# Kernel optimization log

Hardware: AMD Instinct MI355X
Metric: run time of the kernel (lower is better)

The kernel has to match this reference:

```python
import jax, jax.numpy as jnp
import numpy as np
from jax import lax

H_SIZE = 2048; ATT = 512; HEAD = 64
H = H_SIZE // HEAD; HK = ATT // HEAD; G = H // HK
D_DECAY = 96; D_AAA = 96; D_MV = 64; D_GATE = 256
B, T = 1, 2048
EPS = 1e-5 * HEAD  # ln_x eps = 1e-5 * head_size


def setup_inputs() -> dict:
    ks = jax.random.split(jax.random.key(0), 32)
    f = jnp.float32
    rn = lambda k, sh, s: jax.random.normal(k, sh, dtype=f) * s
    return {
        "x": rn(ks[0], (B, T, H_SIZE), 1.0),
        "wkv_state_in": jnp.zeros((B, H, HEAD, HEAD), f),
        "v_first_val": rn(ks[1], (B, T, H_SIZE), 1.0),
        "cos": jax.random.uniform(ks[2], (T, HEAD), dtype=f),
        "sin": jax.random.uniform(ks[3], (T, HEAD), dtype=f),
        "w0": rn(ks[4], (1, 1, H_SIZE), 0.3) - 2.0,
        "w1": rn(ks[5], (H_SIZE, D_DECAY), 0.02),
        "w2": rn(ks[6], (D_DECAY, H_SIZE), 0.05),
        "a0": rn(ks[7], (1, 1, H_SIZE), 0.1),
        "a1": rn(ks[8], (H_SIZE, D_AAA), 0.02),
        "a2": rn(ks[9], (D_AAA, H_SIZE), 0.05),
        "v0": jnp.ones((1, 1, H_SIZE), f),
        "v1": rn(ks[10], (H_SIZE, D_MV), 0.02),
        "v2": rn(ks[11], (D_MV, H_SIZE), 0.05),
        "g1": rn(ks[12], (H_SIZE, D_GATE), 0.02),
        "g2": rn(ks[13], (D_GATE, H_SIZE), 0.05),
        "k_k": jnp.full((1, 1, H_SIZE), 0.85, f),
        "k_a": jnp.ones((1, 1, H_SIZE), f),
        "r_k": rn(ks[14], (H, HEAD), 0.2),
        "q_w": rn(ks[15], (H_SIZE, H_SIZE), 0.02), "q_b": rn(ks[16], (H_SIZE,), 0.02),
        "k_w": rn(ks[17], (ATT, H_SIZE), 0.02), "k_b": rn(ks[18], (ATT,), 0.02),
        "v_w": rn(ks[19], (ATT, H_SIZE), 0.02), "v_b": rn(ks[20], (ATT,), 0.02),
        "o_w": rn(ks[21], (H_SIZE, H_SIZE), 0.02),
        "ln_w": jnp.ones((H_SIZE,), f), "ln_b": jnp.zeros((H_SIZE,), f),
    }


def _rope(x4, cos, sin):
    # x4: [B,T,h,N], cos/sin: [T,N]; HF rotate_half convention
    c = cos[None, :, None, :]; s = sin[None, :, None, :]
    x1, x2 = jnp.split(x4, 2, axis=-1)
    return x4 * c + jnp.concatenate([-x2, x1], axis=-1) * s


def _forward(x, wkv_state_in, v_first_val, cos, sin, w0, w1, w2, a0, a1, a2,
             v0, v1, v2, g1, g2, k_k, k_a, r_k, q_w, q_b, k_w, k_b, v_w, v_b,
             o_w, ln_w, ln_b):
    Bx, Tx, C = x.shape
    r = x @ q_w.T + q_b                                   # [B,T,C]
    w_lora = w0 + jnp.tanh(x @ w1) @ w2                   # [B,T,C]
    k = x @ k_w.T + k_b                                   # [B,T,ATT]
    v = x @ v_w.T + v_b                                   # [B,T,ATT]
    g = jax.nn.sigmoid(x @ g1) @ g2                       # [B,T,C]
    iclr = jax.nn.sigmoid(a0 + (x @ a1) @ a2)             # in-context learning rate

    r4 = _rope(r.reshape(Bx, Tx, H, HEAD), cos, sin)
    k4 = _rope(k.reshape(Bx, Tx, HK, HEAD), cos, sin)
    # GQA expand kv heads to all query heads
    k4 = jnp.repeat(k4, G, axis=2)                        # [B,T,H,N]
    v4 = jnp.repeat(v.reshape(Bx, Tx, HK, HEAD), G, axis=2)
    v = v4.reshape(Bx, Tx, C)
    # v_first residual mix (layer_id > 0)
    v = v + (v_first_val - v) * jax.nn.sigmoid(v0 + (x @ v1) @ v2)
    k = k4.reshape(Bx, Tx, C)
    kk = (k * k_k).reshape(Bx, Tx, H, HEAD)
    kk = kk / jnp.maximum(jnp.linalg.norm(kk, axis=-1, keepdims=True), 1e-12)
    k = k * (1.0 + (iclr - 1.0) * k_a)
    # decay: soft-clamped log-decay then double-exp -> (0,1)
    w = jnp.exp(-jnp.exp(-jax.nn.softplus(-w_lora) - 0.5))

    tm = lambda a: jnp.moveaxis(a.reshape(Bx, Tx, H, HEAD), 1, 0)  # time-major [T,B,H,N]
    seq = (tm(r4.reshape(Bx, Tx, C)), tm(w), tm(k), tm(v),
           jnp.moveaxis(kk, 1, 0), tm(iclr))

    def step(S, inp):
        r_t, w_t, k_t, v_t, kk_t, a_t = inp
        ab = kk_t * a_t
        S = (S * w_t[:, :, None, :]
             + jnp.einsum('bhij,bhj,bhk->bhik', S, -kk_t, ab)
             + v_t[..., None] * k_t[:, :, None, :])
        y = jnp.einsum('bhij,bhj->bhi', S, r_t)
        return S, y

    S_out, ys = lax.scan(step, wkv_state_in.astype(jnp.float32), seq)
    y = jnp.moveaxis(ys, 0, 1)                            # [B,T,H,N]
    # GroupNorm(n_head) per token
    mu = y.mean(-1, keepdims=True)
    var = y.var(-1)[..., None]
    y = (y - mu) / jnp.sqrt(var + EPS)
    y = y.reshape(Bx, Tx, C) * ln_w + ln_b
    # per-head bonus term
    bonus = (r4 * k.reshape(Bx, Tx, H, HEAD) * r_k).sum(-1, keepdims=True) \
            * v.reshape(Bx, Tx, H, HEAD)
    y = y + bonus.reshape(Bx, Tx, C)
    out = (y * g) @ o_w.T
    return out, S_out, v_first_val


def reference(x, wkv_state_in, v_first_val, cos, sin, w0, w1, w2, a0, a1, a2,
              v0, v1, v2, g1, g2, k_k, k_a, r_k, q_w, q_b, k_w, k_b, v_w, v_b,
              o_w, ln_w, ln_b):
    return _forward(x, wkv_state_in, v_first_val, cos, sin, w0, w1, w2, a0, a1,
                    a2, v0, v1, v2, g1, g2, k_k, k_a, r_k, q_w, q_b, k_w, k_b,
                    v_w, v_b, o_w, ln_w, ln_b)
```

## Files before the change

kernel.cpp:

```cpp
#include <hip/hip_runtime.h>
#include <hip/hip_bf16.h>

typedef __hip_bfloat16 bf16;
typedef unsigned int u32;
typedef __attribute__((ext_vector_type(8))) __bf16 bf16x8;
typedef __attribute__((ext_vector_type(4))) float f32x4;
typedef __attribute__((ext_vector_type(8))) short short8;

static constexpr int kT   = 2048;
static constexpr int kC   = 2048;
static constexpr int kAtt = 512;

__device__ __forceinline__ float us2f(unsigned short u) {
    union { float f; unsigned int i; } c; c.i = ((unsigned int)u) << 16; return c.f;
}
__device__ __forceinline__ float toF(float v) { return v; }
__device__ __forceinline__ float toF(bf16 v) { return __bfloat162float(v); }
__device__ __forceinline__ void stO(float* p, float v) { *p = v; }
__device__ __forceinline__ void stO(bf16* p, float v) { *p = __float2bfloat16(v); }
__device__ __forceinline__ unsigned short f2us(float x) {
    return __builtin_bit_cast(unsigned short, __float2bfloat16(x));
}
__device__ __forceinline__ u32 packbf(float lo, float hi) {
    return (u32)f2us(lo) | ((u32)f2us(hi) << 16);
}

__device__ __forceinline__ void ld4(const bf16* p, float r[4]) {
    ushort4 u = *reinterpret_cast<const ushort4*>(p);
    r[0] = us2f(u.x); r[1] = us2f(u.y); r[2] = us2f(u.z); r[3] = us2f(u.w);
}
__device__ __forceinline__ void ld4(const float* p, float r[4]) {
    float4 u = *reinterpret_cast<const float4*>(p);
    r[0] = u.x; r[1] = u.y; r[2] = u.z; r[3] = u.w;
}

__device__ __forceinline__ float wred64(float v) {
    #pragma unroll
    for (int m = 32; m > 0; m >>= 1) v += __shfl_xor(v, m, 64);
    return v;
}

__device__ __forceinline__ void gload_lds16(const bf16* g, void* lds) {
    __builtin_amdgcn_global_load_lds(
        (const __attribute__((address_space(1))) void*)g,
        (__attribute__((address_space(3))) void*)lds, 16, 0, 0);
}

__global__ void detect_kernel(const unsigned short* __restrict__ v0,
                              int* __restrict__ flag) {
    if (threadIdx.x == 0) flag[0] = (v0[0] == 0x3F80) ? 0 : 1;
}

struct ConvDesc { const void* src; void* dst; int n; int b0; };
struct ConvTable { ConvDesc d[12]; };

__global__ __launch_bounds__(256) void conv_all(const int* __restrict__ flag,
                                                ConvTable tab) {
    const bool isf = flag[0] != 0;
    const int bid = blockIdx.x;
    int di = 0;
    #pragma unroll
    for (int k = 1; k < 12; k++) if (bid >= tab.d[k].b0) di = k;
    const ConvDesc d = tab.d[di];
    const int i = ((bid - d.b0) * 256 + threadIdx.x) * 4;
    if (i >= d.n) return;
    float r[4];
    if (isf) ld4((const float*)d.src + i, r);
    else     ld4((const bf16*)d.src + i, r);
    bf16* o = (bf16*)d.dst;
    ushort4 o4 = { f2us(r[0]), f2us(r[1]), f2us(r[2]), f2us(r[3]) };
    *reinterpret_cast<ushort4*>(o + i) = o4;
}

struct TransDesc { const void* src; void* dst; int R, C, b0; };
struct TransTable { TransDesc d[8]; };

__global__ __launch_bounds__(256) void trans_all(const int* __restrict__ flag,
                                                 TransTable tab) {
    const bool isf = flag[0] != 0;
    const int bid = blockIdx.x;
    int di = 0;
    #pragma unroll
    for (int k = 1; k < 8; k++) if (bid >= tab.d[k].b0) di = k;
    const TransDesc d = tab.d[di];
    const int tC = d.C >> 5;
    const int tile = bid - d.b0;
    const int by = tile / tC, bx = tile - by * tC;
    __shared__ float tilebuf[32][33];
    const int r0 = by << 5, c0 = bx << 5;
    const int x = threadIdx.x & 31, y4 = (threadIdx.x >> 5) << 2;
    if (isf) {
        const float* src = (const float*)d.src;
        #pragma unroll
        for (int k = 0; k < 4; k++)
            tilebuf[y4 + k][x] = src[(size_t)(r0 + y4 + k) * d.C + c0 + x];
    } else {
        const bf16* src = (const bf16*)d.src;
        #pragma unroll
        for (int k = 0; k < 4; k++)
            tilebuf[y4 + k][x] = toF(src[(size_t)(r0 + y4 + k) * d.C + c0 + x]);
    }
    __syncthreads();
    bf16* dst = (bf16*)d.dst;
    #pragma unroll
    for (int k = 0; k < 4; k++)
        dst[(size_t)(c0 + y4 + k) * d.R + r0 + x] = __float2bfloat16(tilebuf[x][y4 + k]);
}

template<typename OT, int BM, int BN>
__device__ __forceinline__ void gemm_body(
    bf16* As, bf16* Bs,
    const bf16* __restrict__ A, int lda, const bf16* __restrict__ B,
    const bf16* __restrict__ bias, OT* __restrict__ C,
    int N, int K, int epi)
{
    const int tid = threadIdx.x, lane = tid & 63, wave = tid >> 6;
    const int bm = blockIdx.y * BM, bn = blockIdx.x * BN;
    const int wm = (wave >> 1) * (BM / 2), wn = (wave & 1) * (BN / 2);
    constexpr int FI = BM / 32, FJ = BN / 32;
    f32x4 acc[FI][FJ];
    #pragma unroll
    for (int i = 0; i < FI; i++)
        #pragma unroll
        for (int j = 0; j < FJ; j++) acc[i][j] = (f32x4){0.f, 0.f, 0.f, 0.f};
    const int sr = tid >> 2;
    const int sc = (tid & 3) << 3;
    const int fr = lane & 15;
    const int fk = (lane >> 4) << 3;
    char* AsB = (char*)As + wave * 1024;
    char* BsB = (char*)Bs + wave * 1024;
    for (int k0 = 0; k0 < K; k0 += 32) {
        #pragma unroll
        for (int it = 0; it < BM / 64; it++)
            gload_lds16(A + (size_t)(bm + sr + it * 64) * lda + k0 + sc,
                        AsB + it * 4096);
        #pragma unroll
        for (int it = 0; it < BN / 64; it++)
            gload_lds16(B + (size_t)(bn + sr + it * 64) * K + k0 + sc,
                        BsB + it * 4096);
        __syncthreads();
        bf16x8 af[FI], bg[FJ];
        #pragma unroll
        for (int f = 0; f < FI; f++)
            af[f] = *reinterpret_cast<const bf16x8*>(&As[(wm + f * 16 + fr) * 32 + fk]);
        #pragma unroll
        for (int f = 0; f < FJ; f++)
            bg[f] = *reinterpret_cast<const bf16x8*>(&Bs[(wn + f * 16 + fr) * 32 + fk]);
        #pragma unroll
        for (int fi = 0; fi < FI; fi++)
            #pragma unroll
            for (int fj = 0; fj < FJ; fj++)
                acc[fi][fj] = __builtin_amdgcn_mfma_f32_16x16x32_bf16(
                    af[fi], bg[fj], acc[fi][fj], 0, 0, 0);
        __syncthreads();
    }
    #pragma unroll
    for (int fi = 0; fi < FI; fi++) {
        const int m = bm + wm + fi * 16 + ((lane >> 4) << 2);
        #pragma unroll
        for (int fj = 0; fj < FJ; fj++) {
            const int n = bn + wn + fj * 16 + (lane & 15);
            #pragma unroll
            for (int e = 0; e < 4; e++) {
                float v = acc[fi][fj][e];
                if (epi == 1 || epi == 2 || epi == 3) v += toF(bias[n]);
                if (epi == 2) v = 1.f / (1.f + expf(-v));
                if (epi == 3) {
                    v = 1.f / (1.f + expf(-v));
                    v = 1.f - expf(-0.6065306597126334f * v);
                }
                if (epi == 6) {
                    if (n < 96) v = tanhf(v);
                    else if (n >= 256) v = 1.f / (1.f + expf(-v));
                }
                stO(&C[(size_t)(m + e) * N + n], v);
            }
        }
    }
}

template<typename OT, int EPI, int BM, int BN>
__global__ __launch_bounds__(256) void mfma_nt(
    const bf16* __restrict__ A, int lda, const bf16* __restrict__ B,
    const bf16* __restrict__ bias, OT* __restrict__ C, int N, int K)
{
    __shared__ bf16 As[BM * 32];
    __shared__ bf16 Bs[BN * 32];
    gemm_body<OT, BM, BN>(As, Bs, A, lda, B, bias, C, N, K, EPI);
}

struct L2Desc { const bf16* A; const bf16* B; const bf16* bias; bf16* C; int K; int epi; };
struct L2Table { L2Desc d[4]; };

__global__ __launch_bounds__(256) void lora2_all(L2Table tab) {
    __shared__ bf16 As[128 * 32];
    __shared__ bf16 Bs[128 * 32];
    const L2Desc d = tab.d[blockIdx.z];
    gemm_body<bf16, 128, 128>(As, Bs, d.A, 512, d.B, d.bias, d.C, kC, d.K, d.epi);
}

__global__ __launch_bounds__(256) void out_all(
    const int* __restrict__ flag, const bf16* __restrict__ A,
    const bf16* __restrict__ B, bf16* __restrict__ Cb, float* __restrict__ Cf)
{
    __shared__ bf16 As[128 * 32];
    __shared__ bf16 Bs[128 * 32];
    if (flag[0]) gemm_body<float, 128, 128>(As, Bs, A, kC, B, nullptr, Cf, kC, kC, 0);
    else         gemm_body<bf16, 128, 128>(As, Bs, A, kC, B, nullptr, Cb, kC, kC, 0);
}

template<typename IT>
__device__ __forceinline__ void prep_body(
    const bf16* __restrict__ rkv, const bf16* __restrict__ iclr,
    const bf16* __restrict__ wdec, bf16* __restrict__ vout,
    const IT* __restrict__ vfirst, const IT* __restrict__ cosw,
    const IT* __restrict__ sinw, const IT* __restrict__ kkw,
    const IT* __restrict__ kaw, const IT* __restrict__ rkw,
    uint2* __restrict__ pk, bf16* __restrict__ wr, bf16* __restrict__ coef)
{
    const int lane = threadIdx.x & 63;
    const int b = blockIdx.x;
    const int t0 = (b >> 3) * 2;
    const int h = (b & 7) + ((threadIdx.x >> 6) << 3);
    const int ch = h * 64 + lane;
    const int hk = h >> 2;
    const float kkwv = toF(kkw[ch]);
    const float kawv = toF(kaw[ch]);
    const float rkwv = toF(rkw[ch]);
    const float sign = (lane < 32) ? -1.f : 1.f;
    #pragma unroll
    for (int m = 0; m < 2; m++) {
        const int t = t0 + m;
        const size_t idx = (size_t)t * kC + ch;
        const size_t rbase = (size_t)t * 3072;
        const float c = toF(cosw[t * 64 + lane]);
        const float s = toF(sinw[t * 64 + lane]);
        const float rv = toF(rkv[rbase + ch]);
        const float rp = __shfl_xor(rv, 32, 64);
        const float rr = rv * c + sign * rp * s;
        const float kv = toF(rkv[rbase + 2048 + hk * 64 + lane]);
        const float kp = __shfl_xor(kv, 32, 64);
        const float kr = kv * c + sign * kp * s;
        float kkv = kr * kkwv;
        const float ss = wred64(kkv * kkv);
        kkv *= 1.f / fmaxf(sqrtf(ss), 1e-12f);
        const float a = toF(iclr[idx]);
        const float kf = kr * (1.f + (a - 1.f) * kawv);
        const float ab = kkv * a;
        const float w1m = toF(wdec[idx]);
        const float wrv = (1.f - w1m) * rr;
        const float vv = toF(rkv[rbase + 2560 + hk * 64 + lane]);
        const float vf = vv + (toF(vfirst[idx]) - vv) * toF(vout[idx]);
        const float cf = wred64(rr * kf * rkwv);
        uint2 pv; pv.x = packbf(w1m, kkv); pv.y = packbf(ab, kf);
        pk[idx] = pv;
        wr[idx] = __float2bfloat16(wrv);
        vout[idx] = __float2bfloat16(vf);
        if (lane == 0) coef[t * 32 + h] = __float2bfloat16(cf);
    }
}

__global__ __launch_bounds__(256) void prep_all(
    const int* __restrict__ flag,
    const bf16* __restrict__ rkv, const bf16* __restrict__ iclr,
    const bf16* __restrict__ wdec, bf16* __restrict__ vout,
    const void* vfirst, const void* cosw, const void* sinw,
    const void* kkw, const void* kaw, const void* rkw,
    uint2* __restrict__ pk, bf16* __restrict__ wr, bf16* __restrict__ coef)
{
    if (flag[0]) prep_body<float>(rkv, iclr, wdec, vout, (const float*)vfirst,
        (const float*)cosw, (const float*)sinw, (const float*)kkw,
        (const float*)kaw, (const float*)rkw, pk, wr, coef);
    else prep_body<bf16>(rkv, iclr, wdec, vout, (const bf16*)vfirst,
        (const bf16*)cosw, (const bf16*)sinw, (const bf16*)kkw,
        (const bf16*)kaw, (const bf16*)rkw, pk, wr, coef);
}


__device__ __forceinline__ void mm64(f32x4 acc[4], const bf16* A, const bf16* B,
                                     int wv, int ln) {
    const int fr = ln & 15, fk = (ln >> 4) << 3;
    #pragma unroll
    for (int kc = 0; kc < 2; kc++) {
        bf16x8 af = *reinterpret_cast<const bf16x8*>(&A[(wv * 16 + fr) * 72 + kc * 32 + fk]);
        #pragma unroll
        for (int cf = 0; cf < 4; cf++) {
            bf16x8 bg = *reinterpret_cast<const bf16x8*>(&B[(cf * 16 + fr) * 72 + kc * 32 + fk]);
            acc[cf] = __builtin_amdgcn_mfma_f32_16x16x32_bf16(af, bg, acc[cf], 0, 0, 0);
        }
    }
}

__device__ __forceinline__ void wracc(bf16* dst, f32x4 a[4], int wv, int ln) {
    const int row0 = 16 * wv + ((ln >> 4) << 2), c = ln & 15;
    #pragma unroll
    for (int cf = 0; cf < 4; cf++) {
        const int col = cf * 16 + c;
        #pragma unroll
        for (int e = 0; e < 4; e++)
            dst[(row0 + e) * 72 + col] = __float2bfloat16(a[cf][e]);
    }
}

__device__ __forceinline__ void wmask(bf16* dst, f32x4 a[4], int wv, int ln, int mode) {
    const int row0 = 16 * wv + ((ln >> 4) << 2), c = ln & 15;
    #pragma unroll
    for (int cf = 0; cf < 4; cf++) {
        const int col = cf * 16 + c;
        #pragma unroll
        for (int e = 0; e < 4; e++) {
            const int row = row0 + e;
            float v = a[cf][e];
            if (mode == 2) v = -v;
            const bool keep = (mode == 0) ? (col < row) : (col <= row);
            dst[row * 64 + col] = __float2bfloat16(keep ? v : 0.f);
        }
    }
}

__global__ __launch_bounds__(256) void chunkA(
    const uint2* __restrict__ pk, const bf16* __restrict__ wr,
    const int* __restrict__ flag,
    bf16* __restrict__ kG, bf16* __restrict__ rG, bf16* __restrict__ qmG,
    bf16* __restrict__ mG, bf16* __restrict__ npqG_b, bf16* __restrict__ npqG_f,
    bf16* __restrict__ qqG_b, bf16* __restrict__ qqG_f,
    bf16* __restrict__ invG1, bf16* __restrict__ invG2,
    float* __restrict__ wlG)
{
    __shared__ bf16 bK[64 * 72], bR[64 * 72], bA[64 * 72], bKb[64 * 72];
    __shared__ float Pf[64 * 66];
    __shared__ float Mf[64 * 66];
    __shared__ float Wf[4][16 * 17];
    __shared__ float wl[64];
    const int b = blockIdx.x;
    const int h = b & 31, g = b >> 5;
    const int unit = b;
    const int t0 = g * 64, hb = h * 64;
    const int tid = threadIdx.x, wv = tid >> 6, ln = tid & 63;
    bf16* npqG = flag[0] ? npqG_f : npqG_b;
    bf16* qqG  = flag[0] ? qqG_f  : qqG_b;
    bf16* invG = (unit < 512) ? invG1 + (size_t)unit * 4096
                              : invG2 + (size_t)(unit - 512) * 4096;
    if (tid < 64) {
        const int j = tid;
        const size_t base = (size_t)t0 * kC + hb + j;
        uint2 pr[8]; float wrr[8];
        #pragma unroll
        for (int p = 0; p < 8; p++) {
            pr[p] = pk[base + (size_t)p * kC];
            wrr[p] = toF(wr[base + (size_t)p * kC]);
        }
        float W = 1.f;
        for (int u = 0; u < 64; u++) {
            const int sl = u & 7;
            const uint2 pv = pr[sl]; const float wvv = wrr[sl];
            pr[sl] = pk[base + (size_t)(u + 8) * kC];
            wrr[sl] = toF(wr[base + (size_t)(u + 8) * kC]);
            const float w1m = us2f(pv.x & 0xffff), kk = us2f(pv.x >> 16);
            const float ab  = us2f(pv.y & 0xffff), kf = us2f(pv.y >> 16);
            const float w = 1.f - w1m;
            bK[u * 72 + j] = __float2bfloat16(W * kk);
            bR[u * 72 + j] = __float2bfloat16(W * wvv);
            W *= w;
            const float inv = 1.f / W;
            bA[u * 72 + j]  = __float2bfloat16(ab * inv);
            bKb[u * 72 + j] = __float2bfloat16(kf * inv);
            invG[u * 64 + j] = __float2bfloat16(inv);
        }
        wl[j] = W;
        wlG[unit * 64 + j] = W;
    }
    __syncthreads();
    {
        f32x4 a1[4];
        #pragma unroll
        for (int i = 0; i < 4; i++) a1[i] = (f32x4){0.f, 0.f, 0.f, 0.f};
        mm64(a1, bK, bA, wv, ln);
        const int row0 = 16 * wv + ((ln >> 4) << 2), c = ln & 15;
        #pragma unroll
        for (int cf = 0; cf < 4; cf++)
            #pragma unroll
            for (int e = 0; e < 4; e++)
                Pf[(row0 + e) * 66 + cf * 16 + c] = a1[cf][e];
    }
    {
        f32x4 a2[4];
        #pragma unroll
        for (int i = 0; i < 4; i++) a2[i] = (f32x4){0.f, 0.f, 0.f, 0.f};
        mm64(a2, bK, bKb, wv, ln);
        wmask(qmG + (size_t)unit * 4096, a2, wv, ln, 0);
    }
    {
        f32x4 a3[4];
        #pragma unroll
        for (int i = 0; i < 4; i++) a3[i] = (f32x4){0.f, 0.f, 0.f, 0.f};
        mm64(a3, bR, bA, wv, ln);
        wmask(npqG + (size_t)unit * 4096, a3, wv, ln, 2);
    }
    {
        f32x4 a4[4];
        #pragma unroll
        for (int i = 0; i < 4; i++) a4[i] = (f32x4){0.f, 0.f, 0.f, 0.f};
        mm64(a4, bR, bKb, wv, ln);
        wmask(qqG + (size_t)unit * 4096, a4, wv, ln, 1);
    }
    __syncthreads();
    for (int idx = tid; idx < 4096; idx += 256) {
        const int u = idx >> 6, j = idx & 63;
        kG[(size_t)unit * 4096 + idx] = bK[u * 72 + j];
        rG[(size_t)unit * 4096 + idx] = bR[u * 72 + j];
        Mf[u * 66 + j] = 0.f;
    }
    __syncthreads();
    if (tid < 64) {
        const int bb = tid >> 4, m = tid & 15, b0 = bb * 16;
        float x[16];
        #pragma unroll
        for (int j = 0; j < 16; j++) x[j] = (j == m) ? 1.f : 0.f;
        #pragma unroll
        for (int r = 1; r < 16; r++) {
            float acc = 0.f;
            #pragma unroll
            for (int j = 0; j < r; j++)
                acc += Pf[(b0 + r) * 66 + b0 + j] * x[j];
            x[r] -= acc;
        }
        #pragma unroll
        for (int j = 0; j < 16; j++)
            Mf[(b0 + j) * 66 + b0 + m] = x[j];
    }
    __syncthreads();
    #pragma unroll
    for (int dlev = 1; dlev <= 3; dlev++) {
        const int bi = wv + dlev, bj = wv;
        const bool act = (bi < 4);
        const int c = ln & 15, rg = (ln >> 4) << 2;
        if (act) {
            float w4[4] = {0.f, 0.f, 0.f, 0.f};
            for (int kb = bj; kb < bi; kb++)
                #pragma unroll
                for (int t = 0; t < 16; t++) {
                    const float mv = Mf[(kb * 16 + t) * 66 + bj * 16 + c];
                    #pragma unroll
                    for (int e = 0; e < 4; e++)
                        w4[e] += Pf[(bi * 16 + rg + e) * 66 + kb * 16 + t] * mv;
                }
            #pragma unroll
            for (int e = 0; e < 4; e++) Wf[wv][(rg + e) * 17 + c] = w4[e];
        }
        __syncthreads();
        if (act) {
            float m4[4] = {0.f, 0.f, 0.f, 0.f};
            #pragma unroll
            for (int t = 0; t < 16; t++) {
                const float wvl = Wf[wv][t * 17 + c];
                #pragma unroll
                for (int e = 0; e < 4; e++)
                    m4[e] += Mf[(bi * 16 + rg + e) * 66 + bi * 16 + t] * wvl;
            }
            #pragma unroll
            for (int e = 0; e < 4; e++)
                Mf[(bi * 16 + rg + e) * 66 + bj * 16 + c] = -m4[e];
        }
        __syncthreads();
    }
    for (int idx = tid; idx < 4096; idx += 256) {
        const int mp = idx >> 6, m = idx & 63;
        mG[(size_t)unit * 4096 + idx] = __float2bfloat16(Mf[mp * 66 + m]);
    }
}

__device__ __forceinline__ void stage8k(bf16* dst, const bf16* src, int tid) {
    const int r = tid >> 2, c0 = (tid & 3) << 4;
    short8 a = *reinterpret_cast<const short8*>(&src[r * 64 + c0]);
    short8 b = *reinterpret_cast<const short8*>(&src[r * 64 + c0 + 8]);
    *reinterpret_cast<short8*>(&dst[r * 72 + c0]) = a;
    *reinterpret_cast<short8*>(&dst[r * 72 + c0 + 8]) = b;
}

__global__ __launch_bounds__(256) void stateB1(
    const int* __restrict__ flag,
    uint2* __restrict__ pk, const bf16* __restrict__ vout,
    const bf16* __restrict__ s0,
    const bf16* __restrict__ kG, const bf16* __restrict__ qmG,
    const bf16* __restrict__ mG,
    const bf16* __restrict__ invG1, const bf16* __restrict__ invG2,
    const float* __restrict__ wlG,
    bf16* __restrict__ dG,
    bf16* __restrict__ sout_b, float* __restrict__ sout_f)
{
    __shared__ float Sf[64 * 66];
    __shared__ float wl[64];
    __shared__ bf16 bS[64 * 72], Vb[64 * 72], bE[64 * 72], bD[64 * 72];
    __shared__ bf16 sK[64 * 72], sQM[64 * 72], sM[64 * 72], sINV[64 * 72];
    __shared__ bf16 sNAT[64 * 72], sKT[64 * 72];
    const int h = blockIdx.x, hb = h * 64;
    const int tid = threadIdx.x, wv = tid >> 6, ln = tid & 63;
    const bool isf = flag[0] != 0;
    const int pr = tid >> 2, pc0 = (tid & 3) << 4;
    const int vu = tid >> 6, vr = tid & 63;
    short8 pf[4][2];
    float vrg[16];
    auto issue = [&](int g) {
        const int u_ = (g << 5) | h;
        const size_t ub = (size_t)u_ * 4096;
        const bf16* iv = (u_ < 512) ? invG1 + ub : invG2 + ub - (size_t)512 * 4096;
        pf[0][0] = *reinterpret_cast<const short8*>(kG + ub + pr * 64 + pc0);
        pf[0][1] = *reinterpret_cast<const short8*>(kG + ub + pr * 64 + pc0 + 8);
        pf[1][0] = *reinterpret_cast<const short8*>(qmG + ub + pr * 64 + pc0);
        pf[1][1] = *reinterpret_cast<const short8*>(qmG + ub + pr * 64 + pc0 + 8);
        pf[2][0] = *reinterpret_cast<const short8*>(mG + ub + pr * 64 + pc0);
        pf[2][1] = *reinterpret_cast<const short8*>(mG + ub + pr * 64 + pc0 + 8);
        pf[3][0] = *reinterpret_cast<const short8*>(iv + pr * 64 + pc0);
        pf[3][1] = *reinterpret_cast<const short8*>(iv + pr * 64 + pc0 + 8);
        const int t0_ = g * 64;
        #pragma unroll
        for (int k = 0; k < 16; k++)
            vrg[k] = toF(vout[(size_t)(t0_ + vu + 4 * k) * kC + hb + vr]);
    };
    for (int idx = tid; idx < 4096; idx += 256) {
        const int r = idx >> 6, j = idx & 63;
        Sf[r * 66 + j] = toF(s0[(size_t)(hb + r) * 64 + j]);
    }
    issue(0);
    for (int g = 0; g < 32; g++) {
        const int unit = (g << 5) | h, t0 = g * 64;
        *reinterpret_cast<short8*>(&sK[pr * 72 + pc0])       = pf[0][0];
        *reinterpret_cast<short8*>(&sK[pr * 72 + pc0 + 8])   = pf[0][1];
        *reinterpret_cast<short8*>(&sQM[pr * 72 + pc0])      = pf[1][0];
        *reinterpret_cast<short8*>(&sQM[pr * 72 + pc0 + 8])  = pf[1][1];
        *reinterpret_cast<short8*>(&sM[pr * 72 + pc0])       = pf[2][0];
        *reinterpret_cast<short8*>(&sM[pr * 72 + pc0 + 8])   = pf[2][1];
        *reinterpret_cast<short8*>(&sINV[pr * 72 + pc0])     = pf[3][0];
        *reinterpret_cast<short8*>(&sINV[pr * 72 + pc0 + 8]) = pf[3][1];
        #pragma unroll
        for (int k = 0; k < 16; k++)
            Vb[vr * 72 + vu + 4 * k] = __float2bfloat16(vrg[k]);
        if (tid < 64) wl[tid] = wlG[unit * 64 + tid];
        __syncthreads();
        if (g + 1 < 32) issue(g + 1);
        for (int idx = tid; idx < 4096; idx += 256) {
            const int j = idx & 63, u = idx >> 6;
            const u32 py = pk[(size_t)(t0 + u) * kC + hb + j].y;
            const float ab = us2f(py & 0xffff), kf = us2f(py >> 16);
            const float f = toF(sINV[u * 72 + j]) * wl[j];
            sNAT[j * 72 + u] = __float2bfloat16(-ab * f);
            sKT[j * 72 + u]  = __float2bfloat16(kf * f);
        }
        for (int idx = tid; idx < 4096; idx += 256) {
            const int r = idx >> 6, j = idx & 63;
            const unsigned short sv = f2us(Sf[r * 66 + j]);
            bS[r * 72 + j] = __builtin_bit_cast(bf16, sv);
            reinterpret_cast<unsigned short*>(
                &pk[(size_t)(t0 + r) * kC + hb + j])[0] = sv;
        }
        __syncthreads();
        {
            f32x4 ae[4];
            #pragma unroll
            for (int i = 0; i < 4; i++) ae[i] = (f32x4){0.f, 0.f, 0.f, 0.f};
            mm64(ae, bS, sK, wv, ln);
            mm64(ae, Vb, sQM, wv, ln);
            wracc(bE, ae, wv, ln);
        }
        __syncthreads();
        {
            f32x4 ad[4];
            #pragma unroll
            for (int i = 0; i < 4; i++) ad[i] = (f32x4){0.f, 0.f, 0.f, 0.f};
            mm64(ad, bE, sM, wv, ln);
            wracc(bD, ad, wv, ln);
        }
        __syncthreads();
        for (int idx = tid; idx < 4096; idx += 256)
            dG[(size_t)unit * 4096 + idx] = bD[(idx >> 6) * 72 + (idx & 63)];
        {
            f32x4 as_[4];
            #pragma unroll
            for (int i = 0; i < 4; i++) as_[i] = (f32x4){0.f, 0.f, 0.f, 0.f};
            mm64(as_, bD, sNAT, wv, ln);
            mm64(as_, Vb, sKT, wv, ln);
            const int row0 = 16 * wv + ((ln >> 4) << 2), c = ln & 15;
            #pragma unroll
            for (int cf = 0; cf < 4; cf++) {
                const int col = cf * 16 + c;
                const float wlc = wl[col];
                #pragma unroll
                for (int e = 0; e < 4; e++) {
                    const int r = row0 + e;
                    Sf[r * 66 + col] = Sf[r * 66 + col] * wlc + as_[cf][e];
                }
            }
        }
        __syncthreads();
    }
    for (int idx = tid; idx < 4096; idx += 256) {
        const int r = idx >> 6, j = idx & 63;
        const float v = Sf[r * 66 + j];
        if (isf) sout_f[(size_t)(hb + r) * 64 + j] = v;
        else     sout_b[(size_t)(hb + r) * 64 + j] = __float2bfloat16(v);
    }
}

__global__ __launch_bounds__(256) void ypassB2(
    const int* __restrict__ flag,
    const uint2* __restrict__ pk,
    const bf16* __restrict__ vout,
    const bf16* __restrict__ rG, const bf16* __restrict__ dG,
    const bf16* __restrict__ npqG_b, const bf16* __restrict__ npqG_f,
    const bf16* __restrict__ qqG_b, const bf16* __restrict__ qqG_f,
    bf16* __restrict__ y)
{
    __shared__ bf16 sS[64 * 72], sD[64 * 72], sR[64 * 72];
    __shared__ bf16 sNPq[64 * 72], sQq[64 * 72], Vb[64 * 72];
    const int b = blockIdx.x;
    const int h = b & 31, g = b >> 5;
    const int unit = b, t0 = g * 64, hb = h * 64;
    const int tid = threadIdx.x, wv = tid >> 6, ln = tid & 63;
    const bool isf = flag[0] != 0;
    const bf16* npqG = isf ? npqG_f : npqG_b;
    const bf16* qqG  = isf ? qqG_f  : qqG_b;
    const size_t ub = (size_t)unit * 4096;
    stage8k(sD, dG + ub, tid);
    stage8k(sR, rG + ub, tid);
    stage8k(sNPq, npqG + ub, tid);
    stage8k(sQq, qqG + ub, tid);
    for (int idx = tid; idx < 4096; idx += 256) {
        const int r = idx >> 6, j = idx & 63;
        const uint2 cell = pk[(size_t)(t0 + r) * kC + hb + j];
        sS[r * 72 + j] = __builtin_bit_cast(bf16, (unsigned short)(cell.x & 0xffff));
    }
    for (int idx = tid; idx < 4096; idx += 256) {
        const int u = idx >> 6, r = idx & 63;
        Vb[r * 72 + u] = vout[(size_t)(t0 + u) * kC + hb + r];
    }
    __syncthreads();
    f32x4 ay[4];
    #pragma unroll
    for (int i = 0; i < 4; i++) ay[i] = (f32x4){0.f, 0.f, 0.f, 0.f};
    mm64(ay, sS, sR, wv, ln);
    mm64(ay, sD, sNPq, wv, ln);
    mm64(ay, Vb, sQq, wv, ln);
    const int row0 = 16 * wv + ((ln >> 4) << 2), c = ln & 15;
    #pragma unroll
    for (int cf = 0; cf < 4; cf++) {
        const int col = cf * 16 + c;
        ushort4 o = { f2us(ay[cf][0]), f2us(ay[cf][1]),
                      f2us(ay[cf][2]), f2us(ay[cf][3]) };
        *reinterpret_cast<ushort4*>(&y[(size_t)(t0 + col) * kC + hb + row0]) = o;
    }
}

template<typename IT>
__device__ __forceinline__ void gnorm_body(
    bf16* __restrict__ y, const bf16* __restrict__ coef,
    const bf16* __restrict__ vout, const bf16* __restrict__ gate,
    const IT* __restrict__ lnw, const IT* __restrict__ lnb)
{
    const int gt = blockIdx.x * 256 + threadIdx.x;
    const int lane = gt & 63;
    const int wid = gt >> 6;
    const int t = wid >> 5;
    const int h = wid & 31;
    const int ch = h * 64 + lane;
    const size_t idx = (size_t)t * kC + ch;
    const float yv = toF(y[idx]);
    const float mu = wred64(yv) * (1.f / 64.f);
    const float d = yv - mu;
    const float var = wred64(d * d) * (1.f / 64.f);
    float yo = d * rsqrtf(var + 6.4e-4f);
    yo = yo * toF(lnw[ch]) + toF(lnb[ch]);
    yo += toF(coef[t * 32 + h]) * toF(vout[idx]);
    y[idx] = __float2bfloat16(yo * toF(gate[idx]));
}

__global__ __launch_bounds__(256) void gnorm_all(
    const int* __restrict__ flag, bf16* __restrict__ y,
    const bf16* __restrict__ coef, const bf16* __restrict__ vout,
    const bf16* __restrict__ gate, const void* lnw, const void* lnb,
    const uint4* __restrict__ cpin, uint4* __restrict__ cpout_b,
    uint4* __restrict__ cpout_f, int ncp_b, int ncp_f)
{
    if (blockIdx.x >= 16384) {
        const int i = (blockIdx.x - 16384) * 256 + threadIdx.x;
        if (flag[0]) { if (i < ncp_f) cpout_f[i] = cpin[i]; }
        else         { if (i < ncp_b) cpout_b[i] = cpin[i]; }
        return;
    }
    if (flag[0]) gnorm_body<float>(y, coef, vout, gate,
        (const float*)lnw, (const float*)lnb);
    else gnorm_body<bf16>(y, coef, vout, gate,
        (const bf16*)lnw, (const bf16*)lnb);
}

extern "C" void kernel_launch(void* const* d_in, const int* in_sizes, int n_in,
                              void* d_out, int out_size, void* d_ws, size_t ws_size,
                              hipStream_t stream)
{
    (void)in_sizes; (void)n_in; (void)out_size; (void)ws_size;
    void* const xP   = d_in[0];
    void* const s0P  = d_in[1];
    void* const vfP  = d_in[2];
    void* const cosP = d_in[3];
    void* const sinP = d_in[4];
    void* const w0P  = d_in[5];
    void* const w1P  = d_in[6];
    void* const w2P  = d_in[7];
    void* const a0P  = d_in[8];
    void* const a1P  = d_in[9];
    void* const a2P  = d_in[10];
    void* const v0P  = d_in[11];
    void* const v1P  = d_in[12];
    void* const v2P  = d_in[13];
    void* const g1P  = d_in[14];
    void* const g2P  = d_in[15];
    void* const kkP  = d_in[16];
    void* const kaP  = d_in[17];
    void* const rkP  = d_in[18];
    void* const qwP  = d_in[19];
    void* const qbP  = d_in[20];
    void* const kwP  = d_in[21];
    void* const kbP  = d_in[22];
    void* const vwP  = d_in[23];
    void* const vbP  = d_in[24];
    void* const owP  = d_in[25];
    void* const lnwP = d_in[26];
    void* const lnbP = d_in[27];

    const size_t M4 = 4194304;

    char* W = (char*)d_ws;
    auto alloc = [&](size_t bytes) { char* p = W; W += (bytes + 255) & ~(size_t)255; return (void*)p; };
    int*   flagp = (int*)  alloc(256);
    uint2* pkb   = (uint2*)alloc(M4 * 8);
    bf16*  wrb   = (bf16*) alloc(M4 * 2);
    bf16*  rkv   = (bf16*) alloc((size_t)kT * 3072 * 2);
    bf16*  wdec  = (bf16*) alloc(M4 * 2);
    bf16*  iclr  = (bf16*) alloc(M4 * 2);
    bf16*  vout  = (bf16*) alloc(M4 * 2);
    bf16*  gate  = (bf16*) alloc(M4 * 2);
    bf16*  xb    = (bf16*) alloc(M4 * 2);
    bf16*  qkvw  = (bf16*) alloc((size_t)3072 * 2048 * 2);
    bf16*  owb   = (bf16*) alloc(M4 * 2);
    bf16*  l1w   = (bf16*) alloc((size_t)512 * 2048 * 2);
    bf16*  hcat  = (bf16*) alloc((size_t)2048 * 512 * 2);
    bf16*  w2t   = (bf16*) alloc(2048 * 96 * 2);
    bf16*  a2t   = (bf16*) alloc(2048 * 96 * 2);
    bf16*  v2t   = (bf16*) alloc(2048 * 64 * 2);
    bf16*  g2t   = (bf16*) alloc(2048 * 256 * 2);
    bf16*  qkvb  = (bf16*) alloc(3072 * 2);
    bf16*  w0b   = (bf16*) alloc(2048 * 2);
    bf16*  a0b   = (bf16*) alloc(2048 * 2);
    bf16*  v0b   = (bf16*) alloc(2048 * 2);
    bf16*  s0b   = (bf16*) alloc(131072 * 2);
    u32*   c12   = (u32*)  alloc(kT * 32 * 4);
    bf16*  coefb = (bf16*) alloc(kT * 32 * 2);
    (void)alloc(16384);

    bf16* ybuf = xb;

    bf16*  kappaG = rkv;
    bf16*  rhoG   = wdec;
    bf16*  qmG    = iclr;
    bf16*  mG     = qkvw;
    bf16*  invG1  = qkvw + (size_t)4194304;
    bf16*  invG2  = l1w;
    float* wlG    = (float*)c12;
    bf16*  dG     = wrb;
    bf16* npq_b = (bf16*)d_out;
    bf16* npq_f = (bf16*)d_out;
    bf16* qq_b  = (bf16*)((char*)d_out + (M4 + 131072) * 2);
    bf16* qq_f  = (bf16*)((char*)d_out + (M4 + 131072) * 4);

    dim3 blk(256);

    detect_kernel<<<dim3(1), dim3(64), 0, stream>>>((const unsigned short*)v0P, flagp);

    ConvTable ct;
    ct.d[0]  = { xP,  xb,                         (int)M4,     0 };
    ct.d[1]  = { qwP, qkvw,                       (int)M4,     4096 };
    ct.d[2]  = { kwP, qkvw + (size_t)2048 * 2048, kAtt * kC,   8192 };
    ct.d[3]  = { vwP, qkvw + (size_t)2560 * 2048, kAtt * kC,   9216 };
    ct.d[4]  = { owP, owb,                        (int)M4,     10240 };
    ct.d[5]  = { qbP, qkvb,        2048,   14336 };
    ct.d[6]  = { kbP, qkvb + 2048, 512,    14338 };
    ct.d[7]  = { vbP, qkvb + 2560, 512,    14339 };
    ct.d[8]  = { w0P, w0b, 2048,           14340 };
    ct.d[9]  = { a0P, a0b, 2048,           14342 };
    ct.d[10] = { v0P, v0b, 2048,           14344 };
    ct.d[11] = { s0P, s0b, 131072,         14346 };
    conv_all<<<dim3(14474), blk, 0, stream>>>(flagp, ct);

    TransTable tt;
    tt.d[0] = { w1P, l1w,                       2048, 96,   0 };
    tt.d[1] = { a1P, l1w + (size_t)96 * 2048,   2048, 96,   192 };
    tt.d[2] = { v1P, l1w + (size_t)192 * 2048,  2048, 64,   384 };
    tt.d[3] = { g1P, l1w + (size_t)256 * 2048,  2048, 256,  512 };
    tt.d[4] = { w2P, w2t, 96, 2048,   1024 };
    tt.d[5] = { a2P, a2t, 96, 2048,   1216 };
    tt.d[6] = { v2P, v2t, 64, 2048,   1408 };
    tt.d[7] = { g2P, g2t, 256, 2048,  1536 };
    trans_all<<<dim3(2048), blk, 0, stream>>>(flagp, tt);

    mfma_nt<bf16, 1, 128, 128><<<dim3(24, 16), blk, 0, stream>>>(xb, kC, qkvw, qkvb, rkv, 3072, kC);
    mfma_nt<bf16, 6, 64, 64><<<dim3(8, 32),  blk, 0, stream>>>(xb, kC, l1w, nullptr, hcat, 512, kC);
    L2Table lt;
    lt.d[0] = { hcat,       w2t, w0b,     wdec, 96,  3 };
    lt.d[1] = { hcat + 96,  a2t, a0b,     iclr, 96,  2 };
    lt.d[2] = { hcat + 192, v2t, v0b,     vout, 64,  2 };
    lt.d[3] = { hcat + 256, g2t, nullptr, gate, 256, 0 };
    lora2_all<<<dim3(16, 16, 4), blk, 0, stream>>>(lt);

    prep_all<<<dim3(8192), blk, 0, stream>>>(flagp, rkv, iclr, wdec, vout,
        vfP, cosP, sinP, kkP, kaP, rkP, pkb, wrb, coefb);

    chunkA<<<dim3(1024), blk, 0, stream>>>(pkb, wrb, flagp,
        kappaG, rhoG, qmG, mG, npq_b, npq_f, qq_b, qq_f, invG1, invG2, wlG);

    stateB1<<<dim3(32), blk, 0, stream>>>(flagp, pkb, vout, s0b,
        kappaG, qmG, mG, invG1, invG2, wlG, dG,
        (bf16*)d_out + M4, (float*)d_out + M4);

    ypassB2<<<dim3(1024), blk, 0, stream>>>(flagp, pkb, vout,
        rhoG, dG, npq_b, npq_f, qq_b, qq_f, ybuf);

    gnorm_all<<<dim3(16384 + 4096), blk, 0, stream>>>(flagp, ybuf, coefb,
        vout, gate, lnwP, lnbP,
        (const uint4*)vfP,
        (uint4*)((bf16*)d_out + M4 + 131072),
        (uint4*)((float*)d_out + M4 + 131072),
        (int)(M4 * 2 / 16), (int)(M4 * 4 / 16));

    out_all<<<dim3(16, 16), blk, 0, stream>>>(flagp, ybuf, owb,
        (bf16*)d_out, (float*)d_out);
}
```

Baseline: 655.1 us.

## Split sequential state pass across row groups and precompute transposed decay factors

The sequential chunk-state kernel now runs 128 blocks instead of 32, each block owning 16 of the 64 state rows of one head. Each step therefore does 16x64 MFMA tiles instead of 64x64, which shortens the serial critical path per chunk. The scaled and transposed a/k factors, previously built inside the serial loop from pk and inverse-decay values, are now computed once in chunkA and stored to global memory. The cost is redundant loads of shared K/QM/M/AT/KT tiles by four blocks per head, plus extra global scratch that reuses existing buffers (xb, rkv), which raises aliasing risk.

```diff
diff --git a/kernel.cpp b/kernel.cpp
--- a/kernel.cpp
+++ b/kernel.cpp
@@ -291,15 +291,23 @@
     }
 }
 
-__device__ __forceinline__ void wracc(bf16* dst, f32x4 a[4], int wv, int ln) {
-    const int row0 = 16 * wv + ((ln >> 4) << 2), c = ln & 15;
-    #pragma unroll
-    for (int cf = 0; cf < 4; cf++) {
-        const int col = cf * 16 + c;
-        #pragma unroll
-        for (int e = 0; e < 4; e++)
-            dst[(row0 + e) * 72 + col] = __float2bfloat16(a[cf][e]);
-    }
+__device__ __forceinline__ f32x4 mm16(f32x4 acc, const bf16* A, const bf16* B,
+                                      int wv, int ln) {
+    const int fr = ln & 15, fk = (ln >> 4) << 3;
+    #pragma unroll
+    for (int kc = 0; kc < 2; kc++) {
+        bf16x8 af = *reinterpret_cast<const bf16x8*>(&A[fr * 72 + kc * 32 + fk]);
+        bf16x8 bg = *reinterpret_cast<const bf16x8*>(&B[(wv * 16 + fr) * 72 + kc * 32 + fk]);
+        acc = __builtin_amdgcn_mfma_f32_16x16x32_bf16(af, bg, acc, 0, 0, 0);
+    }
+    return acc;
+}
+
+__device__ __forceinline__ void wracc16(bf16* dst, f32x4 a, int wv, int ln) {
+    const int row0 = (ln >> 4) << 2, c = ln & 15;
+    #pragma unroll
+    for (int e = 0; e < 4; e++)
+        dst[(row0 + e) * 72 + wv * 16 + c] = __float2bfloat16(a[e]);
 }
 
 __device__ __forceinline__ void wmask(bf16* dst, f32x4 a[4], int wv, int ln, int mode) {
@@ -324,7 +332,8 @@
     bf16* __restrict__ kG, bf16* __restrict__ rG, bf16* __restrict__ qmG,
     bf16* __restrict__ mG, bf16* __restrict__ npqG_b, bf16* __restrict__ npqG_f,
     bf16* __restrict__ qqG_b, bf16* __restrict__ qqG_f,
-    bf16* __restrict__ invG1, bf16* __restrict__ invG2,
+    bf16* __restrict__ aht1, bf16* __restrict__ aht2,
+    bf16* __restrict__ kht1, bf16* __restrict__ kht2,
     float* __restrict__ wlG)
 {
     __shared__ bf16 bK[64 * 72], bR[64 * 72], bA[64 * 72], bKb[64 * 72];
@@ -339,8 +348,10 @@
     const int tid = threadIdx.x, wv = tid >> 6, ln = tid & 63;
     bf16* npqG = flag[0] ? npqG_f : npqG_b;
     bf16* qqG  = flag[0] ? qqG_f  : qqG_b;
-    bf16* invG = (unit < 512) ? invG1 + (size_t)unit * 4096
-                              : invG2 + (size_t)(unit - 512) * 4096;
+    bf16* ahtG = (unit < 512) ? aht1 + (size_t)unit * 4096
+                              : aht2 + (size_t)(unit - 512) * 4096;
+    bf16* khtG = (unit < 512) ? kht1 + (size_t)unit * 4096
+                              : kht2 + (size_t)(unit - 512) * 4096;
     if (tid < 64) {
         const int j = tid;
         const size_t base = (size_t)t0 * kC + hb + j;
@@ -365,7 +376,6 @@
             const float inv = 1.f / W;
             bA[u * 72 + j]  = __float2bfloat16(ab * inv);
             bKb[u * 72 + j] = __float2bfloat16(kf * inv);
-            invG[u * 64 + j] = __float2bfloat16(inv);
         }
         wl[j] = W;
         wlG[unit * 64 + j] = W;
@@ -409,6 +419,9 @@
         const int u = idx >> 6, j = idx & 63;
         kG[(size_t)unit * 4096 + idx] = bK[u * 72 + j];
         rG[(size_t)unit * 4096 + idx] = bR[u * 72 + j];
+        const float wlj = wl[j];
+        ahtG[j * 64 + u] = __float2bfloat16(-toF(bA[u * 72 + j]) * wlj);
+        khtG[j * 64 + u] = __float2bfloat16( toF(bKb[u * 72 + j]) * wlj);
         Mf[u * 66 + j] = 0.f;
     }
     __syncthreads();
@@ -484,121 +497,116 @@
     const bf16* __restrict__ s0,
     const bf16* __restrict__ kG, const bf16* __restrict__ qmG,
     const bf16* __restrict__ mG,
-    const bf16* __restrict__ invG1, const bf16* __restrict__ invG2,
+    const bf16* __restrict__ aht1, const bf16* __restrict__ aht2,
+    const bf16* __restrict__ kht1, const bf16* __restrict__ kht2,
     const float* __restrict__ wlG,
     bf16* __restrict__ dG,
     bf16* __restrict__ sout_b, float* __restrict__ sout_f)
 {
-    __shared__ float Sf[64 * 66];
+    __shared__ bf16 sK[64 * 72], sQM[64 * 72], sM[64 * 72];
+    __shared__ bf16 sNAT[64 * 72], sKT[64 * 72];
+    __shared__ bf16 bS[16 * 72], Vb[16 * 72], bE[16 * 72], bD[16 * 72];
+    __shared__ float Sf[16 * 66];
     __shared__ float wl[64];
-    __shared__ bf16 bS[64 * 72], Vb[64 * 72], bE[64 * 72], bD[64 * 72];
-    __shared__ bf16 sK[64 * 72], sQM[64 * 72], sM[64 * 72], sINV[64 * 72];
-    __shared__ bf16 sNAT[64 * 72], sKT[64 * 72];
-    const int h = blockIdx.x, hb = h * 64;
+    const int b = blockIdx.x;
+    const int h = b & 31, rg = b >> 5, hb = h * 64, r0g = rg * 16;
     const int tid = threadIdx.x, wv = tid >> 6, ln = tid & 63;
     const bool isf = flag[0] != 0;
     const int pr = tid >> 2, pc0 = (tid & 3) << 4;
-    const int vu = tid >> 6, vr = tid & 63;
-    short8 pf[4][2];
-    float vrg[16];
+    short8 pf[5][2];
+    float vrg[4];
+    float wlr = 0.f;
     auto issue = [&](int g) {
         const int u_ = (g << 5) | h;
         const size_t ub = (size_t)u_ * 4096;
-        const bf16* iv = (u_ < 512) ? invG1 + ub : invG2 + ub - (size_t)512 * 4096;
+        const bf16* ah = (u_ < 512) ? aht1 + ub : aht2 + ub - (size_t)512 * 4096;
+        const bf16* kh = (u_ < 512) ? kht1 + ub : kht2 + ub - (size_t)512 * 4096;
         pf[0][0] = *reinterpret_cast<const short8*>(kG + ub + pr * 64 + pc0);
         pf[0][1] = *reinterpret_cast<const short8*>(kG + ub + pr * 64 + pc0 + 8);
         pf[1][0] = *reinterpret_cast<const short8*>(qmG + ub + pr * 64 + pc0);
         pf[1][1] = *reinterpret_cast<const short8*>(qmG + ub + pr * 64 + pc0 + 8);
         pf[2][0] = *reinterpret_cast<const short8*>(mG + ub + pr * 64 + pc0);
         pf[2][1] = *reinterpret_cast<const short8*>(mG + ub + pr * 64 + pc0 + 8);
-        pf[3][0] = *reinterpret_cast<const short8*>(iv + pr * 64 + pc0);
-        pf[3][1] = *reinterpret_cast<const short8*>(iv + pr * 64 + pc0 + 8);
-        const int t0_ = g * 64;
-        #pragma unroll
-        for (int k = 0; k < 16; k++)
-            vrg[k] = toF(vout[(size_t)(t0_ + vu + 4 * k) * kC + hb + vr]);
+        pf[3][0] = *reinterpret_cast<const short8*>(ah + pr * 64 + pc0);
+        pf[3][1] = *reinterpret_cast<const short8*>(ah + pr * 64 + pc0 + 8);
+        pf[4][0] = *reinterpret_cast<const short8*>(kh + pr * 64 + pc0);
+        pf[4][1] = *reinterpret_cast<const short8*>(kh + pr * 64 + pc0 + 8);
+        ld4(vout + (size_t)(g * 64 + (tid >> 2)) * kC + hb + r0g + ((tid & 3) << 2), vrg);
+        if (tid < 64) wlr = wlG[u_ * 64 + tid];
     };
-    for (int idx = tid; idx < 4096; idx += 256) {
+    for (int idx = tid; idx < 1024; idx += 256) {
         const int r = idx >> 6, j = idx & 63;
-        Sf[r * 66 + j] = toF(s0[(size_t)(hb + r) * 64 + j]);
+        Sf[r * 66 + j] = toF(s0[(size_t)(hb + r0g + r) * 64 + j]);
     }
     issue(0);
     for (int g = 0; g < 32; g++) {
         const int unit = (g << 5) | h, t0 = g * 64;
-        *reinterpret_cast<short8*>(&sK[pr * 72 + pc0])       = pf[0][0];
-        *reinterpret_cast<short8*>(&sK[pr * 72 + pc0 + 8])   = pf[0][1];
-        *reinterpret_cast<short8*>(&sQM[pr * 72 + pc0])      = pf[1][0];
-        *reinterpret_cast<short8*>(&sQM[pr * 72 + pc0 + 8])  = pf[1][1];
-        *reinterpret_cast<short8*>(&sM[pr * 72 + pc0])       = pf[2][0];
-        *reinterpret_cast<short8*>(&sM[pr * 72 + pc0 + 8])   = pf[2][1];
-        *reinterpret_cast<short8*>(&sINV[pr * 72 + pc0])     = pf[3][0];
-        *reinterpret_cast<short8*>(&sINV[pr * 72 + pc0 + 8]) = pf[3][1];
-        #pragma unroll
-        for (int k = 0; k < 16; k++)
-            Vb[vr * 72 + vu + 4 * k] = __float2bfloat16(vrg[k]);
-        if (tid < 64) wl[tid] = wlG[unit * 64 + tid];
+        *reinterpret_cast<short8*>(&sK[pr * 72 + pc0])        = pf[0][0];
+        *reinterpret_cast<short8*>(&sK[pr * 72 + pc0 + 8])    = pf[0][1];
+        *reinterpret_cast<short8*>(&sQM[pr * 72 + pc0])       = pf[1][0];
+        *reinterpret_cast<short8*>(&sQM[pr * 72 + pc0 + 8])   = pf[1][1];
+        *reinterpret_cast<short8*>(&sM[pr * 72 + pc0])        = pf[2][0];
+        *reinterpret_cast<short8*>(&sM[pr * 72 + pc0 + 8])    = pf[2][1];
+        *reinterpret_cast<short8*>(&sNAT[pr * 72 + pc0])      = pf[3][0];
+        *reinterpret_cast<short8*>(&sNAT[pr * 72 + pc0 + 8])  = pf[3][1];
+        *reinterpret_cast<short8*>(&sKT[pr * 72 + pc0])       = pf[4][0];
+        *reinterpret_cast<short8*>(&sKT[pr * 72 + pc0 + 8])   = pf[4][1];
+        {
+            const int u = tid >> 2, rr = (tid & 3) << 2;
+            #pragma unroll
+            for (int k = 0; k < 4; k++)
+                Vb[(rr + k) * 72 + u] = __float2bfloat16(vrg[k]);
+        }
+        if (tid < 64) wl[tid] = wlr;
+        {
+            const int r = tid >> 4, j0 = (tid & 15) << 2;
+            #pragma unroll
+            for (int k = 0; k < 4; k++) {
+                const unsigned short sv = f2us(Sf[r * 66 + j0 + k]);
+                bS[r * 72 + j0 + k] = __builtin_bit_cast(bf16, sv);
+                reinterpret_cast<unsigned short*>(
+                    &pk[(size_t)(t0 + r0g + r) * kC + hb + j0 + k])[0] = sv;
+            }
+        }
         __syncthreads();
         if (g + 1 < 32) issue(g + 1);
-        for (int idx = tid; idx < 4096; idx += 256) {
-            const int j = idx & 63, u = idx >> 6;
-            const u32 py = pk[(size_t)(t0 + u) * kC + hb + j].y;
-            const float ab = us2f(py & 0xffff), kf = us2f(py >> 16);
-            const float f = toF(sINV[u * 72 + j]) * wl[j];
-            sNAT[j * 72 + u] = __float2bfloat16(-ab * f);
-            sKT[j * 72 + u]  = __float2bfloat16(kf * f);
-        }
-        for (int idx = tid; idx < 4096; idx += 256) {
-            const int r = idx >> 6, j = idx & 63;
-            const unsigned short sv = f2us(Sf[r * 66 + j]);
-            bS[r * 72 + j] = __builtin_bit_cast(bf16, sv);
-            reinterpret_cast<unsigned short*>(
-                &pk[(size_t)(t0 + r) * kC + hb + j])[0] = sv;
+        {
+            f32x4 ae = (f32x4){0.f, 0.f, 0.f, 0.f};
+            ae = mm16(ae, bS, sK, wv, ln);
+            ae = mm16(ae, Vb, sQM, wv, ln);
+            wracc16(bE, ae, wv, ln);
         }
         __syncthreads();
         {
-            f32x4 ae[4];
-            #pragma unroll
-            for (int i = 0; i < 4; i++) ae[i] = (f32x4){0.f, 0.f, 0.f, 0.f};
-            mm64(ae, bS, sK, wv, ln);
-            mm64(ae, Vb, sQM, wv, ln);
-            wracc(bE, ae, wv, ln);
+            f32x4 ad = (f32x4){0.f, 0.f, 0.f, 0.f};
+            ad = mm16(ad, bE, sM, wv, ln);
+            wracc16(bD, ad, wv, ln);
         }
         __syncthreads();
         {
-            f32x4 ad[4];
-            #pragma unroll
-            for (int i = 0; i < 4; i++) ad[i] = (f32x4){0.f, 0.f, 0.f, 0.f};
-            mm64(ad, bE, sM, wv, ln);
-            wracc(bD, ad, wv, ln);
+            f32x4 as_ = (f32x4){0.f, 0.f, 0.f, 0.f};
+            as_ = mm16(as_, bD, sNAT, wv, ln);
+            as_ = mm16(as_, Vb, sKT, wv, ln);
+            const int row0 = (ln >> 4) << 2, c = ln & 15;
+            const int col = wv * 16 + c;
+            const float wlc = wl[col];
+            #pragma unroll
+            for (int e = 0; e < 4; e++)
+                Sf[(row0 + e) * 66 + col] = Sf[(row0 + e) * 66 + col] * wlc + as_[e];
+        }
+        {
+            const int r = tid >> 4, u0 = (tid & 15) << 2;
+            #pragma unroll
+            for (int k = 0; k < 4; k++)
+                dG[(size_t)unit * 4096 + (r0g + r) * 64 + u0 + k] = bD[r * 72 + u0 + k];
         }
         __syncthreads();
-        for (int idx = tid; idx < 4096; idx += 256)
-            dG[(size_t)unit * 4096 + idx] = bD[(idx >> 6) * 72 + (idx & 63)];
-        {
-            f32x4 as_[4];
-            #pragma unroll
-            for (int i = 0; i < 4; i++) as_[i] = (f32x4){0.f, 0.f, 0.f, 0.f};
-            mm64(as_, bD, sNAT, wv, ln);
-            mm64(as_, Vb, sKT, wv, ln);
-            const int row0 = 16 * wv + ((ln >> 4) << 2), c = ln & 15;
-            #pragma unroll
-            for (int cf = 0; cf < 4; cf++) {
-                const int col = cf * 16 + c;
-                const float wlc = wl[col];
-                #pragma unroll
-                for (int e = 0; e < 4; e++) {
-                    const int r = row0 + e;
-                    Sf[r * 66 + col] = Sf[r * 66 + col] * wlc + as_[cf][e];
-                }
-            }
-        }
-        __syncthreads();
-    }
-    for (int idx = tid; idx < 4096; idx += 256) {
+    }
+    for (int idx = tid; idx < 1024; idx += 256) {
         const int r = idx >> 6, j = idx & 63;
         const float v = Sf[r * 66 + j];
-        if (isf) sout_f[(size_t)(hb + r) * 64 + j] = v;
-        else     sout_b[(size_t)(hb + r) * 64 + j] = __float2bfloat16(v);
+        if (isf) sout_f[(size_t)(hb + r0g + r) * 64 + j] = v;
+        else     sout_b[(size_t)(hb + r0g + r) * 64 + j] = __float2bfloat16(v);
     }
 }
 
@@ -760,11 +768,13 @@
     bf16* ybuf = xb;
 
     bf16*  kappaG = rkv;
+    bf16*  kht1   = rkv + (size_t)4194304;
     bf16*  rhoG   = wdec;
     bf16*  qmG    = iclr;
     bf16*  mG     = qkvw;
-    bf16*  invG1  = qkvw + (size_t)4194304;
-    bf16*  invG2  = l1w;
+    bf16*  aht1   = qkvw + (size_t)4194304;
+    bf16*  aht2   = l1w;
+    bf16*  kht2   = xb;
     float* wlG    = (float*)c12;
     bf16*  dG     = wrb;
     bf16* npq_b = (bf16*)d_out;
@@ -815,10 +825,11 @@
         vfP, cosP, sinP, kkP, kaP, rkP, pkb, wrb, coefb);
 
     chunkA<<<dim3(1024), blk, 0, stream>>>(pkb, wrb, flagp,
-        kappaG, rhoG, qmG, mG, npq_b, npq_f, qq_b, qq_f, invG1, invG2, wlG);
-
-    stateB1<<<dim3(32), blk, 0, stream>>>(flagp, pkb, vout, s0b,
-        kappaG, qmG, mG, invG1, invG2, wlG, dG,
+        kappaG, rhoG, qmG, mG, npq_b, npq_f, qq_b, qq_f,
+        aht1, aht2, kht1, kht2, wlG);
+
+    stateB1<<<dim3(128), blk, 0, stream>>>(flagp, pkb, vout, s0b,
+        kappaG, qmG, mG, aht1, aht2, kht1, kht2, wlG, dG,
         (bf16*)d_out + M4, (float*)d_out + M4);
 
     ypassB2<<<dim3(1024), blk, 0, stream>>>(flagp, pkb, vout,
```

After: 547.7 us. 16.4% less time.
